# Performance work log

Hardware: AMD Instinct MI355X
Metric: run time of the kernel (lower is better)

The kernel has to match this reference:

```python
import jax, jax.numpy as jnp
import numpy as np

B, T, F = 512, 512, 16
UNITS = [64, 32, 32, 32]
VOCAB, EDIM = 1281, 4


def setup_inputs() -> dict:
    key = jax.random.key(0)
    ks = jax.random.split(key, 32)
    x = jax.random.normal(ks[0], (B, T, F), jnp.float32)
    # column 1 holds integer org ids (stored as float, as in the TF model)
    ids = jax.random.randint(ks[1], (B, T), 0, VOCAB).astype(jnp.float32)
    x = x.at[:, :, 1].set(ids)
    d = {"input_tensor": x,
         "emb": jax.random.normal(ks[2], (VOCAB, EDIM), jnp.float32) * 0.05}
    din = 1 + (F - 2) + EDIM  # 18
    i = 3
    for l, u in enumerate(UNITS):
        d[f"k{l}"] = jax.random.normal(ks[i], (din, 3 * u), jnp.float32) * 0.1; i += 1
        d[f"r{l}"] = jax.random.normal(ks[i], (u, 3 * u), jnp.float32) * 0.1; i += 1
        d[f"bi{l}"] = jnp.zeros((3 * u,), jnp.float32)
        d[f"bh{l}"] = jnp.zeros((3 * u,), jnp.float32)
        din = u
    u = UNITS[-1]
    d["w1"] = jax.random.normal(ks[i], (u, u), jnp.float32) * 0.1; i += 1
    d["b1"] = jnp.zeros((u,), jnp.float32)
    d["w2"] = jax.random.normal(ks[i], (u, u), jnp.float32) * 0.1; i += 1
    d["b2"] = jnp.zeros((u,), jnp.float32)
    d["v"] = jax.random.normal(ks[i], (u, 1), jnp.float32) * 0.1; i += 1
    d["bv"] = jnp.zeros((1,), jnp.float32)
    d["wd"] = jax.random.normal(ks[i], (u, 2), jnp.float32) * 0.1; i += 1
    d["bd"] = jnp.zeros((2,), jnp.float32)
    return d


def _gru(h, xp, rk, bh):
    # Keras GRUCell (reset_after=True). xp = x @ kernel + input_bias, [B, 3u]
    hp = h @ rk + bh
    xz, xr, xh = jnp.split(xp, 3, axis=-1)
    hz, hr, hhp = jnp.split(hp, 3, axis=-1)
    z = jax.nn.sigmoid(xz + hz)
    r = jax.nn.sigmoid(xr + hr)
    hh = jnp.tanh(xh + r * hhp)
    return z * h + (1.0 - z) * hh


def _forward(input_tensor, emb, k0, r0, bi0, bh0, k1, r1, bi1, bh1,
             k2, r2, bi2, bh2, k3, r3, bi3, bh3,
             w1, b1, w2, b2, v, bv, wd, bd):
    f0 = input_tensor[:, :, :1]                      # [B,T,1]
    ids = input_tensor[:, :, 1].astype(jnp.int32)    # [B,T]
    rest = input_tensor[:, :, 2:]                    # [B,T,F-2]
    e = emb[ids]                                     # [B,T,4]
    inp = jnp.concatenate([f0, rest, e], axis=2)     # [B,T,din]

    # precompute layer-0 input projection as one big GEMM
    xp0 = inp @ k0 + bi0                             # [B,T,3*64]
    bsz = inp.shape[0]
    init = tuple(jnp.zeros((bsz, u), inp.dtype) for u in UNITS)

    def step(carry, xp_t):
        h0, h1, h2, h3 = carry
        h0 = _gru(h0, xp_t, r0, bh0)
        h1 = _gru(h1, h0 @ k1 + bi1, r1, bh1)
        h2 = _gru(h2, h1 @ k2 + bi2, r2, bh2)
        h3 = _gru(h3, h2 @ k3 + bi3, r3, bh3)
        return (h0, h1, h2, h3), h3

    (_, _, _, hT), seq = jax.lax.scan(step, init, jnp.swapaxes(xp0, 0, 1))
    outputs = jnp.swapaxes(seq, 0, 1)                # [B,T,32] (last-layer sequence)

    # Bahdanau attention: query = final state of last layer
    score = jnp.tanh(outputs @ w1 + b1 + (hT @ w2 + b2)[:, None, :]) @ v + bv  # [B,T,1]
    attn = jax.nn.softmax(score, axis=1)
    ctx = jnp.sum(attn * outputs, axis=1)            # [B,32]
    return jax.nn.softmax(ctx @ wd + bd, axis=-1)    # [B,2]


def reference(input_tensor, emb, k0, r0, bi0, bh0, k1, r1, bi1, bh1,
              k2, r2, bi2, bh2, k3, r3, bi3, bh3,
              w1, b1, w2, b2, v, bv, wd, bd):
    return _forward(input_tensor, emb, k0, r0, bi0, bh0, k1, r1, bi1, bh1,
                    k2, r2, bi2, bh2, k3, r3, bi3, bh3,
                    w1, b1, w2, b2, v, bv, wd, bd)
```

## Files before the change

### kernel.cpp

```cpp
#include <hip/hip_runtime.h>

#define TLEN 512
#define FIN 16

__device__ __forceinline__ float sigm(float x) { return 1.0f / (1.0f + __expf(-x)); }
__device__ __forceinline__ float tanh_f(float x) {
  x = fminf(fmaxf(x, -15.0f), 15.0f);
  float e = __expf(2.0f * x);
  return (e - 1.0f) / (e + 1.0f);
}

__device__ __forceinline__ float gru_fin(float own_main, float own_xh, float own_hhp,
                                         int role, float hold) {
  const float oth_main = __shfl_xor(own_main, 1);
  const float xh  = own_xh  + __shfl_xor(own_xh, 1);
  const float hhp = own_hhp + __shfl_xor(own_hhp, 1);
  const float sz = role ? oth_main : own_main;
  const float sr = role ? own_main : oth_main;
  const float z = sigm(sz);
  const float r = sigm(sr);
  const float hh = tanh_f(xh + r * hhp);
  return z * hold + (1.f - z) * hh;
}

__global__ __launch_bounds__(256, 1)
void rnn_pipe3(const float* __restrict__ x, const float* __restrict__ emb,
               const float* __restrict__ k0, const float* __restrict__ r0,
               const float* __restrict__ bi0, const float* __restrict__ bh0,
               const float* __restrict__ k1, const float* __restrict__ r1,
               const float* __restrict__ bi1, const float* __restrict__ bh1,
               const float* __restrict__ k2, const float* __restrict__ r2,
               const float* __restrict__ bi2, const float* __restrict__ bh2,
               const float* __restrict__ k3, const float* __restrict__ r3,
               const float* __restrict__ bi3, const float* __restrict__ bh3,
               const float* __restrict__ w1, const float* __restrict__ b1,
               const float* __restrict__ w2, const float* __restrict__ b2,
               const float* __restrict__ vv, const float* __restrict__ bv,
               const float* __restrict__ wd, const float* __restrict__ bd,
               float* __restrict__ out, float* __restrict__ obuf)
{
  __shared__ __align__(16) float s_xin[TLEN][20][2];
  __shared__ __align__(16) float s_h0[2][64][2];
  __shared__ __align__(16) float s_h1[2][32][2];
  __shared__ __align__(16) float s_h2[2][32][2];
  __shared__ __align__(16) float s_h3[2][32][2];
  __shared__ __align__(16) float s_pA[2][64][2];
  __shared__ __align__(16) float s_pAh[2][64][2];
  __shared__ __align__(16) float s_fl[2][16][2][32];
  __shared__ __align__(16) float e_w1[1024];
  __shared__ __align__(16) float e_sc[1024];
  __shared__ float e_hw2[64], e_b1[32], e_v[32], e_ctx[64];

  const int tid  = threadIdx.x;
  const int wid  = tid >> 6;
  const int lane = tid & 63;
  const int g    = lane >> 1;
  const int role = lane & 1;
  const int bb0  = blockIdx.x * 2;

  float Wa[96], Wb[48], Wc[48];
  float bm = 0.f, bxh = 0.f, bhh = 0.f;
  float cbm = 0.f, cbxh = 0.f, cbhh = 0.f;

  if (wid <= 1) {
    const int u  = wid * 32 + g;
    const int cm = role ? 64 + u : u;
    #pragma unroll
    for (int j = 0; j < 19; ++j) Wa[j] = k0[j*192 + cm];
    Wa[19] = 0.f;
    #pragma unroll
    for (int j = 0; j < 64; ++j) Wa[20+j] = r0[j*192 + cm];
    #pragma unroll
    for (int jj = 0; jj < 10; ++jj) {
      const int row = role*10 + jj;
      Wb[jj] = (row < 19) ? k0[row*192 + 128 + u] : 0.f;
    }
    #pragma unroll
    for (int jj = 0; jj < 32; ++jj) Wb[10+jj] = r0[(role*32+jj)*192 + 128 + u];
    bm  = bi0[cm] + bh0[cm];
    bxh = role ? 0.f : bi0[128+u];
    bhh = role ? bh0[128+u] : 0.f;
  }
  if (wid == 0) {
    const int cma = role ? 32 + g : g;
    #pragma unroll
    for (int j = 0; j < 32; ++j) Wc[j] = k3[j*96 + cma];
    #pragma unroll
    for (int jj = 0; jj < 16; ++jj) Wc[32+jj] = k3[(role*16+jj)*96 + 64 + g];
  }
  if (wid == 2) {
    const int cm = role ? 32 + g : g;
    #pragma unroll
    for (int j = 0; j < 64; ++j) Wa[j] = k1[j*96 + cm];
    #pragma unroll
    for (int j = 0; j < 32; ++j) Wa[64+j] = r1[j*96 + cm];
    #pragma unroll
    for (int jj = 0; jj < 32; ++jj) Wb[jj] = k1[(role*32+jj)*96 + 64 + g];
    #pragma unroll
    for (int jj = 0; jj < 16; ++jj) Wb[32+jj] = r1[(role*16+jj)*96 + 64 + g];
    bm  = bi1[cm] + bh1[cm];
    bxh = role ? 0.f : bi1[64+g];
    bhh = role ? bh1[64+g] : 0.f;
  }
  if (wid == 3) {
    const int cm = role ? 32 + g : g;
    #pragma unroll
    for (int j = 0; j < 32; ++j) Wa[j] = k2[j*96 + cm];
    #pragma unroll
    for (int j = 0; j < 32; ++j) Wa[32+j] = r2[j*96 + cm];
    #pragma unroll
    for (int jj = 0; jj < 16; ++jj) Wb[jj] = k2[(role*16+jj)*96 + 64 + g];
    #pragma unroll
    for (int jj = 0; jj < 16; ++jj) Wb[16+jj] = r2[(role*16+jj)*96 + 64 + g];
    bm  = bi2[cm] + bh2[cm];
    bxh = role ? 0.f : bi2[64+g];
    bhh = role ? bh2[64+g] : 0.f;
    #pragma unroll
    for (int j = 0; j < 32; ++j) Wc[j] = r3[j*96 + cm];
    #pragma unroll
    for (int jj = 0; jj < 16; ++jj) Wc[32+jj] = r3[(role*16+jj)*96 + 64 + g];
    cbm  = bi3[cm] + bh3[cm];
    cbxh = bi3[64+g];
    cbhh = bh3[64+g];
  }

  ((float*)s_h0)[tid] = 0.f;
  if (tid < 128) {
    ((float*)s_h1)[tid] = 0.f;
    ((float*)s_h2)[tid] = 0.f;
    ((float*)s_h3)[tid] = 0.f;
  }

  for (int r = tid; r < 2*TLEN; r += 256) {
    const int b2 = r & 1, t2 = r >> 1;
    const float* xr = &x[((size_t)(bb0+b2)*TLEN + t2)*FIN];
    const float4 x0 = *(const float4*)(xr);
    const float4 x1 = *(const float4*)(xr+4);
    const float4 x2 = *(const float4*)(xr+8);
    const float4 x3 = *(const float4*)(xr+12);
    float v[20];
    v[0]=x0.x; v[1]=x0.z; v[2]=x0.w;
    v[3]=x1.x; v[4]=x1.y; v[5]=x1.z; v[6]=x1.w;
    v[7]=x2.x; v[8]=x2.y; v[9]=x2.z; v[10]=x2.w;
    v[11]=x3.x; v[12]=x3.y; v[13]=x3.z; v[14]=x3.w;
    const int id = (int)x0.y;
    const float4 e4 = *(const float4*)&emb[id*4];
    v[15]=e4.x; v[16]=e4.y; v[17]=e4.z; v[18]=e4.w; v[19]=0.f;
    #pragma unroll
    for (int j = 0; j < 20; ++j) s_xin[t2][j][b2] = v[j];
  }

  auto flush = [&](int c) {
    const int par = c & 1;
    #pragma unroll
    for (int it = 0; it < 4; ++it) {
      const int f4 = it*64 + lane;
      const int u4 = f4 & 7, row = f4 >> 3;
      const int dt = row >> 1, b2 = row & 1;
      const float4 vq = *(const float4*)&s_fl[par][dt][b2][u4*4];
      *(float4*)&obuf[(((size_t)(bb0+b2)*TLEN) + c*16 + dt)*32 + u4*4] = vq;
    }
  };

  for (int i = 0; i < 516; ++i) {
    __syncthreads();
    const int wp = i & 1;
    const int rp = wp ^ 1;

    if (wid <= 1) {
      if (i < 512) {
        const int u = wid*32 + g;
        float a0A = bm, a0B = bm, a1A = 0.f, a1B = 0.f;
        #pragma unroll
        for (int j = 0; j < 20; j += 2) {
          const float4 q = *(const float4*)&s_xin[i][j][0];
          a0A += Wa[j]*q.x;   a0B += Wa[j]*q.y;
          a1A += Wa[j+1]*q.z; a1B += Wa[j+1]*q.w;
        }
        #pragma unroll
        for (int j = 0; j < 64; j += 2) {
          const float4 q = *(const float4*)&s_h0[rp][j][0];
          a0A += Wa[20+j]*q.x; a0B += Wa[20+j]*q.y;
          a1A += Wa[21+j]*q.z; a1B += Wa[21+j]*q.w;
        }
        float xqA = bxh, xqB = bxh;
        #pragma unroll
        for (int jj = 0; jj < 10; ++jj) {
          const float2 d = *(const float2*)&s_xin[i][role*10+jj][0];
          xqA += Wb[jj]*d.x; xqB += Wb[jj]*d.y;
        }
        float p0A = bhh, p0B = bhh, p1A = 0.f, p1B = 0.f;
        #pragma unroll
        for (int jj = 0; jj < 32; jj += 2) {
          const float4 q = *(const float4*)&s_h0[rp][role*32+jj][0];
          p0A += Wb[10+jj]*q.x; p0B += Wb[10+jj]*q.y;
          p1A += Wb[11+jj]*q.z; p1B += Wb[11+jj]*q.w;
        }
        const float holdA = s_h0[rp][u][0];
        const float holdB = s_h0[rp][u][1];
        const float hnA = gru_fin(a0A+a1A, xqA, p0A+p1A, role, holdA);
        const float hnB = gru_fin(a0B+a1B, xqB, p0B+p1B, role, holdB);
        if (!role) { s_h0[wp][u][0] = hnA; s_h0[wp][u][1] = hnB; }
      }
      if (wid == 0) {
        if (i >= 3 && i <= 514) {
          float q0A=0.f,q0B=0.f,q1A=0.f,q1B=0.f;
          #pragma unroll
          for (int j = 0; j < 32; j += 2) {
            const float4 q = *(const float4*)&s_h2[rp][j][0];
            q0A += Wc[j]*q.x;   q0B += Wc[j]*q.y;
            q1A += Wc[j+1]*q.z; q1B += Wc[j+1]*q.w;
          }
          float phA=0.f, phB=0.f, ph1A=0.f, ph1B=0.f;
          #pragma unroll
          for (int jj = 0; jj < 16; jj += 2) {
            const float4 q = *(const float4*)&s_h2[rp][role*16+jj][0];
            phA  += Wc[32+jj]*q.x; phB  += Wc[32+jj]*q.y;
            ph1A += Wc[33+jj]*q.z; ph1B += Wc[33+jj]*q.w;
          }
          s_pA[wp][lane][0]  = q0A+q1A;  s_pA[wp][lane][1]  = q0B+q1B;
          s_pAh[wp][lane][0] = phA+ph1A; s_pAh[wp][lane][1] = phB+ph1B;
        }
      } else {
        if (i >= 20 && ((i - 20) & 15) == 0) flush((i - 20) >> 4);
      }
    } else if (wid == 2) {
      if (i >= 1 && i <= 512) {
        float a0A = bm, a0B = bm, a1A=0.f, a1B=0.f;
        #pragma unroll
        for (int j = 0; j < 64; j += 2) {
          const float4 q = *(const float4*)&s_h0[rp][j][0];
          a0A += Wa[j]*q.x;   a0B += Wa[j]*q.y;
          a1A += Wa[j+1]*q.z; a1B += Wa[j+1]*q.w;
        }
        #pragma unroll
        for (int j = 0; j < 32; j += 2) {
          const float4 q = *(const float4*)&s_h1[rp][j][0];
          a0A += Wa[64+j]*q.x; a0B += Wa[64+j]*q.y;
          a1A += Wa[65+j]*q.z; a1B += Wa[65+j]*q.w;
        }
        float x0A = bxh, x0B = bxh, x1A = 0.f, x1B = 0.f;
        #pragma unroll
        for (int jj = 0; jj < 32; jj += 2) {
          const float4 q = *(const float4*)&s_h0[rp][role*32+jj][0];
          x0A += Wb[jj]*q.x;   x0B += Wb[jj]*q.y;
          x1A += Wb[jj+1]*q.z; x1B += Wb[jj+1]*q.w;
        }
        float p0A = bhh, p0B = bhh, p1A = 0.f, p1B = 0.f;
        #pragma unroll
        for (int jj = 0; jj < 16; jj += 2) {
          const float4 q = *(const float4*)&s_h1[rp][role*16+jj][0];
          p0A += Wb[32+jj]*q.x; p0B += Wb[32+jj]*q.y;
          p1A += Wb[33+jj]*q.z; p1B += Wb[33+jj]*q.w;
        }
        const float holdA = s_h1[rp][g][0];
        const float holdB = s_h1[rp][g][1];
        const float hnA = gru_fin(a0A+a1A, x0A+x1A, p0A+p1A, role, holdA);
        const float hnB = gru_fin(a0B+a1B, x0B+x1B, p0B+p1B, role, holdB);
        if (!role) { s_h1[wp][g][0] = hnA; s_h1[wp][g][1] = hnB; }
      }
    } else {
      if (i >= 2 && i <= 513) {
        float a0A = bm, a0B = bm, a1A=0.f, a1B=0.f;
        #pragma unroll
        for (int j = 0; j < 32; j += 2) {
          const float4 q = *(const float4*)&s_h1[rp][j][0];
          a0A += Wa[j]*q.x;   a0B += Wa[j]*q.y;
          a1A += Wa[j+1]*q.z; a1B += Wa[j+1]*q.w;
        }
        #pragma unroll
        for (int j = 0; j < 32; j += 2) {
          const float4 q = *(const float4*)&s_h2[rp][j][0];
          a0A += Wa[32+j]*q.x; a0B += Wa[32+j]*q.y;
          a1A += Wa[33+j]*q.z; a1B += Wa[33+j]*q.w;
        }
        float x0A = bxh, x0B = bxh, x1A = 0.f, x1B = 0.f;
        #pragma unroll
        for (int jj = 0; jj < 16; jj += 2) {
          const float4 q = *(const float4*)&s_h1[rp][role*16+jj][0];
          x0A += Wb[jj]*q.x;   x0B += Wb[jj]*q.y;
          x1A += Wb[jj+1]*q.z; x1B += Wb[jj+1]*q.w;
        }
        float p0A = bhh, p0B = bhh, p1A = 0.f, p1B = 0.f;
        #pragma unroll
        for (int jj = 0; jj < 16; jj += 2) {
          const float4 q = *(const float4*)&s_h2[rp][role*16+jj][0];
          p0A += Wb[16+jj]*q.x; p0B += Wb[16+jj]*q.y;
          p1A += Wb[17+jj]*q.z; p1B += Wb[17+jj]*q.w;
        }
        const float holdA = s_h2[rp][g][0];
        const float holdB = s_h2[rp][g][1];
        const float hnA = gru_fin(a0A+a1A, x0A+x1A, p0A+p1A, role, holdA);
        const float hnB = gru_fin(a0B+a1B, x0B+x1B, p0B+p1B, role, holdB);
        if (!role) { s_h2[wp][g][0] = hnA; s_h2[wp][g][1] = hnB; }
      }
      if (i >= 4) {
        float q0A=0.f,q0B=0.f,q1A=0.f,q1B=0.f;
        #pragma unroll
        for (int jj = 0; jj < 32; jj += 2) {
          const float4 q = *(const float4*)&s_h3[rp][jj][0];
          q0A += Wc[jj]*q.x;   q0B += Wc[jj]*q.y;
          q1A += Wc[jj+1]*q.z; q1B += Wc[jj+1]*q.w;
        }
        float ph0A=0.f, ph0B=0.f, ph1A=0.f, ph1B=0.f;
        #pragma unroll
        for (int jj = 0; jj < 16; jj += 2) {
          const float4 q = *(const float4*)&s_h3[rp][role*16+jj][0];
          ph0A += Wc[32+jj]*q.x; ph0B += Wc[32+jj]*q.y;
          ph1A += Wc[33+jj]*q.z; ph1B += Wc[33+jj]*q.w;
        }
        const float mainA = s_pA[rp][lane][0] + q0A + q1A + cbm;
        const float mainB = s_pA[rp][lane][1] + q0B + q1B + cbm;
        const float xhA_own = s_pAh[rp][lane][0];
        const float xhB_own = s_pAh[rp][lane][1];
        const float phA_own = ph0A + ph1A;
        const float phB_own = ph0B + ph1B;

        const float othA = __shfl_xor(mainA, 1);
        const float othB = __shfl_xor(mainB, 1);
        const float xhA = xhA_own + __shfl_xor(xhA_own, 1) + cbxh;
        const float xhB = xhB_own + __shfl_xor(xhB_own, 1) + cbxh;
        const float hhpA = phA_own + __shfl_xor(phA_own, 1) + cbhh;
        const float hhpB = phB_own + __shfl_xor(phB_own, 1) + cbhh;

        const float szA = role ? othA : mainA;
        const float srA = role ? mainA : othA;
        const float szB = role ? othB : mainB;
        const float srB = role ? mainB : othB;
        const float zA = sigm(szA), rA = sigm(srA);
        const float zB = sigm(szB), rB = sigm(srB);
        const float hhA = tanh_f(xhA + rA*hhpA);
        const float hhB = tanh_f(xhB + rB*hhpB);
        const float hnA = zA*s_h3[rp][g][0] + (1.f-zA)*hhA;
        const float hnB = zB*s_h3[rp][g][1] + (1.f-zB)*hhB;
        if (!role) {
          s_h3[wp][g][0] = hnA;
          s_h3[wp][g][1] = hnB;
          const int t3 = i - 4;
          s_fl[(t3>>4)&1][t3&15][0][g] = hnA;
          s_fl[(t3>>4)&1][t3&15][1][g] = hnB;
        }
      }
    }
  }
  __syncthreads();

  if (wid == 1) flush(31);

  for (int kk = tid; kk < 1024; kk += 256) e_w1[kk] = w1[kk];
  if (tid < 32) { e_b1[tid] = b1[tid]; e_v[tid] = vv[tid]; }
  if (tid >= 64 && tid < 128) {
    const int u = tid & 31, bb = (tid - 64) >> 5;
    float s = b2[u];
    #pragma unroll
    for (int j = 0; j < 32; ++j) s += s_h3[1][j][bb] * w2[j*32 + u];
    e_hw2[bb*32 + u] = s;
  }
  __syncthreads();

  #pragma unroll
  for (int c = 0; c < 4; ++c) {
    const int idx = c*256 + tid;
    const int bb = idx >> 9, t2 = idx & 511;
    const float* row = obuf + ((size_t)(bb0+bb)*TLEN + t2)*32;
    float rr[32];
    #pragma unroll
    for (int j = 0; j < 32; j += 4) {
      const float4 r4 = *(const float4*)&row[j];
      rr[j]=r4.x; rr[j+1]=r4.y; rr[j+2]=r4.z; rr[j+3]=r4.w;
    }
    float sc = 0.f;
    for (int u = 0; u < 32; ++u) {
      float qv = e_b1[u] + e_hw2[bb*32 + u];
      #pragma unroll
      for (int j = 0; j < 32; ++j) qv += rr[j]*e_w1[j*32+u];
      sc += tanh_f(qv)*e_v[u];
    }
    e_sc[idx] = sc;
  }
  __syncthreads();

  {
    if (wid < 2) {
      const int bb = wid;
      float sv[8]; float m = -1e30f;
      #pragma unroll
      for (int k = 0; k < 8; ++k) { sv[k] = e_sc[bb*512 + lane + 64*k]; m = fmaxf(m, sv[k]); }
      #pragma unroll
      for (int off = 32; off > 0; off >>= 1) m = fmaxf(m, __shfl_xor(m, off));
      float ss = 0.f;
      #pragma unroll
      for (int k = 0; k < 8; ++k) { sv[k] = __expf(sv[k]-m); ss += sv[k]; }
      #pragma unroll
      for (int off = 32; off > 0; off >>= 1) ss += __shfl_xor(ss, off);
      const float inv = 1.f/ss;
      #pragma unroll
      for (int k = 0; k < 8; ++k) e_sc[bb*512 + lane + 64*k] = sv[k]*inv;
    }
  }
  __syncthreads();

  if (tid < 64) {
    const int u = tid & 31, bb = tid >> 5;
    float acc = 0.f;
    const float* orow = obuf + (size_t)(bb0+bb)*TLEN*32 + u;
    const float* prow = e_sc + bb*512;
    #pragma unroll 4
    for (int t2 = 0; t2 < 512; ++t2) acc += prow[t2]*orow[(size_t)t2*32];
    e_ctx[bb*32 + u] = acc;
  }
  __syncthreads();

  if (tid < 2) {
    const int bb = tid;
    float l0 = bd[0], l1 = bd[1];
    #pragma unroll
    for (int u = 0; u < 32; ++u) {
      const float cv = e_ctx[bb*32 + u];
      l0 += cv*wd[u*2]; l1 += cv*wd[u*2+1];
    }
    const float mm = fmaxf(l0, l1);
    const float ex0 = __expf(l0-mm), ex1 = __expf(l1-mm);
    const float den = ex0 + ex1;
    out[(bb0+bb)*2 + 0] = ex0/den;
    out[(bb0+bb)*2 + 1] = ex1/den;
  }
}

extern "C" void kernel_launch(void* const* d_in, const int* in_sizes, int n_in,
                              void* d_out, int out_size, void* d_ws, size_t ws_size,
                              hipStream_t stream) {
  const float* x   = (const float*)d_in[0];
  const float* emb = (const float*)d_in[1];
  const float* k0  = (const float*)d_in[2];
  const float* r0  = (const float*)d_in[3];
  const float* bi0 = (const float*)d_in[4];
  const float* bh0 = (const float*)d_in[5];
  const float* k1  = (const float*)d_in[6];
  const float* r1  = (const float*)d_in[7];
  const float* bi1 = (const float*)d_in[8];
  const float* bh1 = (const float*)d_in[9];
  const float* k2  = (const float*)d_in[10];
  const float* r2  = (const float*)d_in[11];
  const float* bi2 = (const float*)d_in[12];
  const float* bh2 = (const float*)d_in[13];
  const float* k3  = (const float*)d_in[14];
  const float* r3  = (const float*)d_in[15];
  const float* bi3 = (const float*)d_in[16];
  const float* bh3 = (const float*)d_in[17];
  const float* w1  = (const float*)d_in[18];
  const float* b1  = (const float*)d_in[19];
  const float* w2  = (const float*)d_in[20];
  const float* b2  = (const float*)d_in[21];
  const float* v   = (const float*)d_in[22];
  const float* bv  = (const float*)d_in[23];
  const float* wd  = (const float*)d_in[24];
  const float* bd  = (const float*)d_in[25];

  float* out  = (float*)d_out;
  float* obuf = (float*)d_ws;

  rnn_pipe3<<<dim3(256), dim3(256), 0, stream>>>(
      x, emb, k0, r0, bi0, bh0, k1, r1, bi1, bh1,
      k2, r2, bi2, bh2, k3, r3, bi3, bh3,
      w1, b1, w2, b2, v, bv, wd, bd, out, obuf);
}
```

Baseline: 1.252 ms.

## Replace per-step block barriers with LDS flag-based dataflow between layer wavefronts

Swaps the lockstep __syncthreads-per-timestep schedule for a producer/consumer dataflow. Each wavefront spins on volatile LDS flags and publishes its progress through an 8-deep ring of hidden-state buffers. The layer-3 work that used to be split across wave 0 and wave 3 now runs entirely in wave 3, and hidden states are carried in registers. This lets layers run ahead of one another instead of waiting on the slowest wave every step. In exchange it adds spin-wait overhead, a longer serial chain in wave 3, and the risk of memory-ordering bugs in the flag protocol.

After: 1.506 ms. 1.2x slower.

```diff
diff --git a/kernel.cpp b/kernel.cpp
--- a/kernel.cpp
+++ b/kernel.cpp
@@ -24,29 +24,28 @@
 }
 
 __global__ __launch_bounds__(256, 1)
-void rnn_pipe3(const float* __restrict__ x, const float* __restrict__ emb,
-               const float* __restrict__ k0, const float* __restrict__ r0,
-               const float* __restrict__ bi0, const float* __restrict__ bh0,
-               const float* __restrict__ k1, const float* __restrict__ r1,
-               const float* __restrict__ bi1, const float* __restrict__ bh1,
-               const float* __restrict__ k2, const float* __restrict__ r2,
-               const float* __restrict__ bi2, const float* __restrict__ bh2,
-               const float* __restrict__ k3, const float* __restrict__ r3,
-               const float* __restrict__ bi3, const float* __restrict__ bh3,
-               const float* __restrict__ w1, const float* __restrict__ b1,
-               const float* __restrict__ w2, const float* __restrict__ b2,
-               const float* __restrict__ vv, const float* __restrict__ bv,
-               const float* __restrict__ wd, const float* __restrict__ bd,
-               float* __restrict__ out, float* __restrict__ obuf)
+void rnn_flow(const float* __restrict__ x, const float* __restrict__ emb,
+              const float* __restrict__ k0, const float* __restrict__ r0,
+              const float* __restrict__ bi0, const float* __restrict__ bh0,
+              const float* __restrict__ k1, const float* __restrict__ r1,
+              const float* __restrict__ bi1, const float* __restrict__ bh1,
+              const float* __restrict__ k2, const float* __restrict__ r2,
+              const float* __restrict__ bi2, const float* __restrict__ bh2,
+              const float* __restrict__ k3, const float* __restrict__ r3,
+              const float* __restrict__ bi3, const float* __restrict__ bh3,
+              const float* __restrict__ w1m, const float* __restrict__ b1,
+              const float* __restrict__ w2m, const float* __restrict__ b2,
+              const float* __restrict__ vv, const float* __restrict__ bv,
+              const float* __restrict__ wd, const float* __restrict__ bd,
+              float* __restrict__ out, float* __restrict__ obuf)
 {
   __shared__ __align__(16) float s_xin[TLEN][20][2];
-  __shared__ __align__(16) float s_h0[2][64][2];
-  __shared__ __align__(16) float s_h1[2][32][2];
-  __shared__ __align__(16) float s_h2[2][32][2];
-  __shared__ __align__(16) float s_h3[2][32][2];
-  __shared__ __align__(16) float s_pA[2][64][2];
-  __shared__ __align__(16) float s_pAh[2][64][2];
-  __shared__ __align__(16) float s_fl[2][16][2][32];
+  __shared__ __align__(16) float s_h0[8][64][2];
+  __shared__ __align__(16) float s_h1[8][32][2];
+  __shared__ __align__(16) float s_h2[8][32][2];
+  __shared__ __align__(16) float s_h3[8][32][2];
+  __shared__ __align__(16) float s_fl[4][16][2][32];
+  __shared__ int s_flag[8];
   __shared__ __align__(16) float e_w1[1024];
   __shared__ __align__(16) float e_sc[1024];
   __shared__ float e_hw2[64], e_b1[32], e_v[32], e_ctx[64];
@@ -58,7 +57,15 @@
   const int role = lane & 1;
   const int bb0  = blockIdx.x * 2;
 
-  float Wa[96], Wb[48], Wc[48];
+#define WAITGE(idx, val) do { volatile int* _f = &s_flag[idx];                 \
+    while (*_f < (val)) {} asm volatile("" ::: "memory"); } while (0)
+#define WAITGE2(i0, i1, val) do { volatile int* _a = &s_flag[i0];              \
+    volatile int* _b = &s_flag[i1];                                            \
+    while (*_a < (val) || *_b < (val)) {} asm volatile("" ::: "memory"); } while (0)
+#define PUBLISH(idx, val) do { asm volatile("s_waitcnt lgkmcnt(0)" ::: "memory"); \
+    if (lane == 0) { *(volatile int*)&s_flag[idx] = (val); } } while (0)
+
+  float W[192];
   float bm = 0.f, bxh = 0.f, bhh = 0.f;
   float cbm = 0.f, cbxh = 0.f, cbhh = 0.f;
 
@@ -66,78 +73,70 @@
     const int u  = wid * 32 + g;
     const int cm = role ? 64 + u : u;
     #pragma unroll
-    for (int j = 0; j < 19; ++j) Wa[j] = k0[j*192 + cm];
-    Wa[19] = 0.f;
-    #pragma unroll
-    for (int j = 0; j < 64; ++j) Wa[20+j] = r0[j*192 + cm];
+    for (int j = 0; j < 19; ++j) W[j] = k0[j*192 + cm];
+    W[19] = 0.f;
+    #pragma unroll
+    for (int j = 0; j < 64; ++j) W[20+j] = r0[j*192 + cm];
     #pragma unroll
     for (int jj = 0; jj < 10; ++jj) {
       const int row = role*10 + jj;
-      Wb[jj] = (row < 19) ? k0[row*192 + 128 + u] : 0.f;
-    }
-    #pragma unroll
-    for (int jj = 0; jj < 32; ++jj) Wb[10+jj] = r0[(role*32+jj)*192 + 128 + u];
+      W[84+jj] = (row < 19) ? k0[row*192 + 128 + u] : 0.f;
+    }
+    #pragma unroll
+    for (int jj = 0; jj < 32; ++jj) W[94+jj] = r0[(role*32+jj)*192 + 128 + u];
     bm  = bi0[cm] + bh0[cm];
     bxh = role ? 0.f : bi0[128+u];
     bhh = role ? bh0[128+u] : 0.f;
-  }
-  if (wid == 0) {
-    const int cma = role ? 32 + g : g;
-    #pragma unroll
-    for (int j = 0; j < 32; ++j) Wc[j] = k3[j*96 + cma];
-    #pragma unroll
-    for (int jj = 0; jj < 16; ++jj) Wc[32+jj] = k3[(role*16+jj)*96 + 64 + g];
-  }
-  if (wid == 2) {
+  } else if (wid == 2) {
     const int cm = role ? 32 + g : g;
     #pragma unroll
-    for (int j = 0; j < 64; ++j) Wa[j] = k1[j*96 + cm];
-    #pragma unroll
-    for (int j = 0; j < 32; ++j) Wa[64+j] = r1[j*96 + cm];
-    #pragma unroll
-    for (int jj = 0; jj < 32; ++jj) Wb[jj] = k1[(role*32+jj)*96 + 64 + g];
-    #pragma unroll
-    for (int jj = 0; jj < 16; ++jj) Wb[32+jj] = r1[(role*16+jj)*96 + 64 + g];
+    for (int j = 0; j < 64; ++j) W[j] = k1[j*96 + cm];
+    #pragma unroll
+    for (int j = 0; j < 32; ++j) W[64+j] = r1[j*96 + cm];
+    #pragma unroll
+    for (int jj = 0; jj < 32; ++jj) W[96+jj]  = k1[(role*32+jj)*96 + 64 + g];
+    #pragma unroll
+    for (int jj = 0; jj < 16; ++jj) W[128+jj] = r1[(role*16+jj)*96 + 64 + g];
     bm  = bi1[cm] + bh1[cm];
     bxh = role ? 0.f : bi1[64+g];
     bhh = role ? bh1[64+g] : 0.f;
-  }
-  if (wid == 3) {
+  } else {
     const int cm = role ? 32 + g : g;
     #pragma unroll
-    for (int j = 0; j < 32; ++j) Wa[j] = k2[j*96 + cm];
-    #pragma unroll
-    for (int j = 0; j < 32; ++j) Wa[32+j] = r2[j*96 + cm];
-    #pragma unroll
-    for (int jj = 0; jj < 16; ++jj) Wb[jj] = k2[(role*16+jj)*96 + 64 + g];
-    #pragma unroll
-    for (int jj = 0; jj < 16; ++jj) Wb[16+jj] = r2[(role*16+jj)*96 + 64 + g];
+    for (int j = 0; j < 32; ++j) { W[j] = k2[j*96 + cm]; W[32+j] = r2[j*96 + cm]; }
+    #pragma unroll
+    for (int jj = 0; jj < 16; ++jj) {
+      W[64+jj] = k2[(role*16+jj)*96 + 64 + g];
+      W[80+jj] = r2[(role*16+jj)*96 + 64 + g];
+    }
+    #pragma unroll
+    for (int j = 0; j < 32; ++j) { W[96+j] = k3[j*96 + cm]; W[128+j] = r3[j*96 + cm]; }
+    #pragma unroll
+    for (int jj = 0; jj < 16; ++jj) {
+      W[160+jj] = k3[(role*16+jj)*96 + 64 + g];
+      W[176+jj] = r3[(role*16+jj)*96 + 64 + g];
+    }
     bm  = bi2[cm] + bh2[cm];
     bxh = role ? 0.f : bi2[64+g];
     bhh = role ? bh2[64+g] : 0.f;
-    #pragma unroll
-    for (int j = 0; j < 32; ++j) Wc[j] = r3[j*96 + cm];
-    #pragma unroll
-    for (int jj = 0; jj < 16; ++jj) Wc[32+jj] = r3[(role*16+jj)*96 + 64 + g];
     cbm  = bi3[cm] + bh3[cm];
     cbxh = bi3[64+g];
     cbhh = bh3[64+g];
   }
 
-  ((float*)s_h0)[tid] = 0.f;
-  if (tid < 128) {
-    ((float*)s_h1)[tid] = 0.f;
-    ((float*)s_h2)[tid] = 0.f;
-    ((float*)s_h3)[tid] = 0.f;
-  }
+  for (int q = tid; q < 1024; q += 256) ((float*)s_h0)[q] = 0.f;
+  for (int q = tid; q < 512; q += 256) {
+    ((float*)s_h1)[q] = 0.f; ((float*)s_h2)[q] = 0.f; ((float*)s_h3)[q] = 0.f;
+  }
+  if (tid < 8) s_flag[tid] = (tid == 4) ? 0 : -1;
 
   for (int r = tid; r < 2*TLEN; r += 256) {
     const int b2 = r & 1, t2 = r >> 1;
-    const float* xr = &x[((size_t)(bb0+b2)*TLEN + t2)*FIN];
+    const float* xr = &x[((size_t)(bb0 + b2) * TLEN + t2) * FIN];
     const float4 x0 = *(const float4*)(xr);
-    const float4 x1 = *(const float4*)(xr+4);
-    const float4 x2 = *(const float4*)(xr+8);
-    const float4 x3 = *(const float4*)(xr+12);
+    const float4 x1 = *(const float4*)(xr + 4);
+    const float4 x2 = *(const float4*)(xr + 8);
+    const float4 x3 = *(const float4*)(xr + 12);
     float v[20];
     v[0]=x0.x; v[1]=x0.z; v[2]=x0.w;
     v[3]=x1.x; v[4]=x1.y; v[5]=x1.z; v[6]=x1.w;
@@ -149,9 +148,10 @@
     #pragma unroll
     for (int j = 0; j < 20; ++j) s_xin[t2][j][b2] = v[j];
   }
+  __syncthreads();
 
   auto flush = [&](int c) {
-    const int par = c & 1;
+    const int par = c & 3;
     #pragma unroll
     for (int it = 0; it < 4; ++it) {
       const int f4 = it*64 + lane;
@@ -162,167 +162,175 @@
     }
   };
 
-  for (int i = 0; i < 516; ++i) {
-    __syncthreads();
-    const int wp = i & 1;
-    const int rp = wp ^ 1;
-
-    if (wid <= 1) {
-      if (i < 512) {
-        const int u = wid*32 + g;
+  if (wid <= 1) {
+    const int u = wid*32 + g;
+    const int FWD = wid ^ 1;
+    float holdA = 0.f, holdB = 0.f;
+    for (int t = 0; t < TLEN; ++t) {
+      if ((t & 3) == 0) WAITGE(2, t - 4);
+      WAITGE(FWD, t - 1);
+      const int sl = t & 7, slp = (t - 1) & 7;
+      float a0A = bm, a0B = bm, a1A = 0.f, a1B = 0.f;
+      #pragma unroll
+      for (int j = 0; j < 20; j += 2) {
+        const float4 q = *(const float4*)&s_xin[t][j][0];
+        a0A += W[j]*q.x;   a0B += W[j]*q.y;
+        a1A += W[j+1]*q.z; a1B += W[j+1]*q.w;
+      }
+      #pragma unroll
+      for (int j = 0; j < 64; j += 2) {
+        const float4 q = *(const float4*)&s_h0[slp][j][0];
+        a0A += W[20+j]*q.x; a0B += W[20+j]*q.y;
+        a1A += W[21+j]*q.z; a1B += W[21+j]*q.w;
+      }
+      float xqA = bxh, xqB = bxh;
+      #pragma unroll
+      for (int jj = 0; jj < 10; ++jj) {
+        const float2 d = *(const float2*)&s_xin[t][role*10+jj][0];
+        xqA += W[84+jj]*d.x; xqB += W[84+jj]*d.y;
+      }
+      float p0A = bhh, p0B = bhh, p1A = 0.f, p1B = 0.f;
+      #pragma unroll
+      for (int jj = 0; jj < 32; jj += 2) {
+        const float4 q = *(const float4*)&s_h0[slp][role*32+jj][0];
+        p0A += W[94+jj]*q.x; p0B += W[94+jj]*q.y;
+        p1A += W[95+jj]*q.z; p1B += W[95+jj]*q.w;
+      }
+      const float hnA = gru_fin(a0A+a1A, xqA, p0A+p1A, role, holdA);
+      const float hnB = gru_fin(a0B+a1B, xqB, p0B+p1B, role, holdB);
+      holdA = hnA; holdB = hnB;
+      if (!role) { s_h0[sl][u][0] = hnA; s_h0[sl][u][1] = hnB; }
+      PUBLISH(wid, t);
+      if (wid == 1 && t >= 20 && ((t - 20) & 15) == 0) {
+        const int c = (t - 20) >> 4;
+        WAITGE(3, 16*c + 16);
+        flush(c);
+        PUBLISH(4, c + 1);
+      }
+    }
+    if (wid == 1) {
+      WAITGE(3, TLEN);
+      flush(31);
+      PUBLISH(4, 32);
+    }
+  } else if (wid == 2) {
+    float holdA = 0.f, holdB = 0.f;
+    for (int t = 0; t < TLEN; ++t) {
+      if ((t & 3) == 0) WAITGE(3, t - 4);
+      WAITGE2(0, 1, t);
+      const int sl = t & 7, slp = (t - 1) & 7;
+      float a0A = bm, a0B = bm, a1A = 0.f, a1B = 0.f;
+      #pragma unroll
+      for (int j = 0; j < 64; j += 2) {
+        const float4 q = *(const float4*)&s_h0[sl][j][0];
+        a0A += W[j]*q.x;   a0B += W[j]*q.y;
+        a1A += W[j+1]*q.z; a1B += W[j+1]*q.w;
+      }
+      #pragma unroll
+      for (int j = 0; j < 32; j += 2) {
+        const float4 q = *(const float4*)&s_h1[slp][j][0];
+        a0A += W[64+j]*q.x; a0B += W[64+j]*q.y;
+        a1A += W[65+j]*q.z; a1B += W[65+j]*q.w;
+      }
+      float x0A = bxh, x0B = bxh, x1A = 0.f, x1B = 0.f;
+      #pragma unroll
+      for (int jj = 0; jj < 32; jj += 2) {
+        const float4 q = *(const float4*)&s_h0[sl][role*32+jj][0];
+        x0A += W[96+jj]*q.x; x0B += W[96+jj]*q.y;
+        x1A += W[97+jj]*q.z; x1B += W[97+jj]*q.w;
+      }
+      float p0A = bhh, p0B = bhh, p1A = 0.f, p1B = 0.f;
+      #pragma unroll
+      for (int jj = 0; jj < 16; jj += 2) {
+        const float4 q = *(const float4*)&s_h1[slp][role*16+jj][0];
+        p0A += W[128+jj]*q.x; p0B += W[128+jj]*q.y;
+        p1A += W[129+jj]*q.z; p1B += W[129+jj]*q.w;
+      }
+      const float hnA = gru_fin(a0A+a1A, x0A+x1A, p0A+p1A, role, holdA);
+      const float hnB = gru_fin(a0B+a1B, x0B+x1B, p0B+p1B, role, holdB);
+      holdA = hnA; holdB = hnB;
+      if (!role) { s_h1[sl][g][0] = hnA; s_h1[sl][g][1] = hnB; }
+      PUBLISH(2, t);
+    }
+  } else {
+    float hold2A = 0.f, hold2B = 0.f, hold3A = 0.f, hold3B = 0.f;
+    for (int j = 0; j <= TLEN; ++j) {
+      if ((j & 15) == 0) WAITGE(4, (j >> 4) - 3);
+      if (j < TLEN) {
+        WAITGE(2, j);
+        const int sl = j & 7, slp = (j - 1) & 7;
         float a0A = bm, a0B = bm, a1A = 0.f, a1B = 0.f;
         #pragma unroll
-        for (int j = 0; j < 20; j += 2) {
-          const float4 q = *(const float4*)&s_xin[i][j][0];
-          a0A += Wa[j]*q.x;   a0B += Wa[j]*q.y;
-          a1A += Wa[j+1]*q.z; a1B += Wa[j+1]*q.w;
-        }
-        #pragma unroll
-        for (int j = 0; j < 64; j += 2) {
-          const float4 q = *(const float4*)&s_h0[rp][j][0];
-          a0A += Wa[20+j]*q.x; a0B += Wa[20+j]*q.y;
-          a1A += Wa[21+j]*q.z; a1B += Wa[21+j]*q.w;
-        }
-        float xqA = bxh, xqB = bxh;
-        #pragma unroll
-        for (int jj = 0; jj < 10; ++jj) {
-          const float2 d = *(const float2*)&s_xin[i][role*10+jj][0];
-          xqA += Wb[jj]*d.x; xqB += Wb[jj]*d.y;
+        for (int jq = 0; jq < 32; jq += 2) {
+          const float4 q = *(const float4*)&s_h1[sl][jq][0];
+          a0A += W[jq]*q.x;   a0B += W[jq]*q.y;
+          a1A += W[jq+1]*q.z; a1B += W[jq+1]*q.w;
+        }
+        #pragma unroll
+        for (int jq = 0; jq < 32; jq += 2) {
+          const float4 q = *(const float4*)&s_h2[slp][jq][0];
+          a0A += W[32+jq]*q.x; a0B += W[32+jq]*q.y;
+          a1A += W[33+jq]*q.z; a1B += W[33+jq]*q.w;
+        }
+        float x0A = bxh, x0B = bxh, x1A = 0.f, x1B = 0.f;
+        #pragma unroll
+        for (int jj = 0; jj < 16; jj += 2) {
+          const float4 q = *(const float4*)&s_h1[sl][role*16+jj][0];
+          x0A += W[64+jj]*q.x; x0B += W[64+jj]*q.y;
+          x1A += W[65+jj]*q.z; x1B += W[65+jj]*q.w;
         }
         float p0A = bhh, p0B = bhh, p1A = 0.f, p1B = 0.f;
         #pragma unroll
-        for (int jj = 0; jj < 32; jj += 2) {
-          const float4 q = *(const float4*)&s_h0[rp][role*32+jj][0];
-          p0A += Wb[10+jj]*q.x; p0B += Wb[10+jj]*q.y;
-          p1A += Wb[11+jj]*q.z; p1B += Wb[11+jj]*q.w;
-        }
-        const float holdA = s_h0[rp][u][0];
-        const float holdB = s_h0[rp][u][1];
-        const float hnA = gru_fin(a0A+a1A, xqA, p0A+p1A, role, holdA);
-        const float hnB = gru_fin(a0B+a1B, xqB, p0B+p1B, role, holdB);
-        if (!role) { s_h0[wp][u][0] = hnA; s_h0[wp][u][1] = hnB; }
-      }
-      if (wid == 0) {
-        if (i >= 3 && i <= 514) {
-          float q0A=0.f,q0B=0.f,q1A=0.f,q1B=0.f;
-          #pragma unroll
-          for (int j = 0; j < 32; j += 2) {
-            const float4 q = *(const float4*)&s_h2[rp][j][0];
-            q0A += Wc[j]*q.x;   q0B += Wc[j]*q.y;
-            q1A += Wc[j+1]*q.z; q1B += Wc[j+1]*q.w;
-          }
-          float phA=0.f, phB=0.f, ph1A=0.f, ph1B=0.f;
-          #pragma unroll
-          for (int jj = 0; jj < 16; jj += 2) {
-            const float4 q = *(const float4*)&s_h2[rp][role*16+jj][0];
-            phA  += Wc[32+jj]*q.x; phB  += Wc[32+jj]*q.y;
-            ph1A += Wc[33+jj]*q.z; ph1B += Wc[33+jj]*q.w;
-          }
-          s_pA[wp][lane][0]  = q0A+q1A;  s_pA[wp][lane][1]  = q0B+q1B;
-          s_pAh[wp][lane][0] = phA+ph1A; s_pAh[wp][lane][1] = phB+ph1B;
-        }
-      } else {
-        if (i >= 20 && ((i - 20) & 15) == 0) flush((i - 20) >> 4);
-      }
-    } else if (wid == 2) {
-      if (i >= 1 && i <= 512) {
-        float a0A = bm, a0B = bm, a1A=0.f, a1B=0.f;
-        #pragma unroll
-        for (int j = 0; j < 64; j += 2) {
-          const float4 q = *(const float4*)&s_h0[rp][j][0];
-          a0A += Wa[j]*q.x;   a0B += Wa[j]*q.y;
-          a1A += Wa[j+1]*q.z; a1B += Wa[j+1]*q.w;
-        }
-        #pragma unroll
-        for (int j = 0; j < 32; j += 2) {
-          const float4 q = *(const float4*)&s_h1[rp][j][0];
-          a0A += Wa[64+j]*q.x; a0B += Wa[64+j]*q.y;
-          a1A += Wa[65+j]*q.z; a1B += Wa[65+j]*q.w;
-        }
-        float x0A = bxh, x0B = bxh, x1A = 0.f, x1B = 0.f;
-        #pragma unroll
-        for (int jj = 0; jj < 32; jj += 2) {
-          const float4 q = *(const float4*)&s_h0[rp][role*32+jj][0];
-          x0A += Wb[jj]*q.x;   x0B += Wb[jj]*q.y;
-          x1A += Wb[jj+1]*q.z; x1B += Wb[jj+1]*q.w;
-        }
-        float p0A = bhh, p0B = bhh, p1A = 0.f, p1B = 0.f;
-        #pragma unroll
         for (int jj = 0; jj < 16; jj += 2) {
-          const float4 q = *(const float4*)&s_h1[rp][role*16+jj][0];
-          p0A += Wb[32+jj]*q.x; p0B += Wb[32+jj]*q.y;
-          p1A += Wb[33+jj]*q.z; p1B += Wb[33+jj]*q.w;
-        }
-        const float holdA = s_h1[rp][g][0];
-        const float holdB = s_h1[rp][g][1];
-        const float hnA = gru_fin(a0A+a1A, x0A+x1A, p0A+p1A, role, holdA);
-        const float hnB = gru_fin(a0B+a1B, x0B+x1B, p0B+p1B, role, holdB);
-        if (!role) { s_h1[wp][g][0] = hnA; s_h1[wp][g][1] = hnB; }
-      }
-    } else {
-      if (i >= 2 && i <= 513) {
-        float a0A = bm, a0B = bm, a1A=0.f, a1B=0.f;
-        #pragma unroll
-        for (int j = 0; j < 32; j += 2) {
-          const float4 q = *(const float4*)&s_h1[rp][j][0];
-          a0A += Wa[j]*q.x;   a0B += Wa[j]*q.y;
-          a1A += Wa[j+1]*q.z; a1B += Wa[j+1]*q.w;
-        }
-        #pragma unroll
-        for (int j = 0; j < 32; j += 2) {
-          const float4 q = *(const float4*)&s_h2[rp][j][0];
-          a0A += Wa[32+j]*q.x; a0B += Wa[32+j]*q.y;
-          a1A += Wa[33+j]*q.z; a1B += Wa[33+j]*q.w;
-        }
-        float x0A = bxh, x0B = bxh, x1A = 0.f, x1B = 0.f;
+          const float4 q = *(const float4*)&s_h2[slp][role*16+jj][0];
+          p0A += W[80+jj]*q.x; p0B += W[80+jj]*q.y;
+          p1A += W[81+jj]*q.z; p1B += W[81+jj]*q.w;
+        }
+        const float hnA = gru_fin(a0A+a1A, x0A+x1A, p0A+p1A, role, hold2A);
+        const float hnB = gru_fin(a0B+a1B, x0B+x1B, p0B+p1B, role, hold2B);
+        hold2A = hnA; hold2B = hnB;
+        if (!role) { s_h2[sl][g][0] = hnA; s_h2[sl][g][1] = hnB; }
+      }
+      if (j >= 1) {
+        const int t3 = j - 1;
+        const int s3 = t3 & 7, s3p = (t3 - 1) & 7;
+        float q0A=0.f,q0B=0.f,q1A=0.f,q1B=0.f;
+        #pragma unroll
+        for (int jq = 0; jq < 32; jq += 2) {
+          const float4 q = *(const float4*)&s_h2[s3][jq][0];
+          q0A += W[96+jq]*q.x; q0B += W[96+jq]*q.y;
+          q1A += W[97+jq]*q.z; q1B += W[97+jq]*q.w;
+        }
+        #pragma unroll
+        for (int jq = 0; jq < 32; jq += 2) {
+          const float4 q = *(const float4*)&s_h3[s3p][jq][0];
+          q0A += W[128+jq]*q.x; q0B += W[128+jq]*q.y;
+          q1A += W[129+jq]*q.z; q1B += W[129+jq]*q.w;
+        }
+        float xh0A=0.f,xh0B=0.f,xh1A=0.f,xh1B=0.f;
         #pragma unroll
         for (int jj = 0; jj < 16; jj += 2) {
-          const float4 q = *(const float4*)&s_h1[rp][role*16+jj][0];
-          x0A += Wb[jj]*q.x;   x0B += Wb[jj]*q.y;
-          x1A += Wb[jj+1]*q.z; x1B += Wb[jj+1]*q.w;
-        }
-        float p0A = bhh, p0B = bhh, p1A = 0.f, p1B = 0.f;
+          const float4 q = *(const float4*)&s_h2[s3][role*16+jj][0];
+          xh0A += W[160+jj]*q.x; xh0B += W[160+jj]*q.y;
+          xh1A += W[161+jj]*q.z; xh1B += W[161+jj]*q.w;
+        }
+        float ph0A=0.f,ph0B=0.f,ph1A=0.f,ph1B=0.f;
         #pragma unroll
         for (int jj = 0; jj < 16; jj += 2) {
-          const float4 q = *(const float4*)&s_h2[rp][role*16+jj][0];
-          p0A += Wb[16+jj]*q.x; p0B += Wb[16+jj]*q.y;
-          p1A += Wb[17+jj]*q.z; p1B += Wb[17+jj]*q.w;
-        }
-        const float holdA = s_h2[rp][g][0];
-        const float holdB = s_h2[rp][g][1];
-        const float hnA = gru_fin(a0A+a1A, x0A+x1A, p0A+p1A, role, holdA);
-        const float hnB = gru_fin(a0B+a1B, x0B+x1B, p0B+p1B, role, holdB);
-        if (!role) { s_h2[wp][g][0] = hnA; s_h2[wp][g][1] = hnB; }
-      }
-      if (i >= 4) {
-        float q0A=0.f,q0B=0.f,q1A=0.f,q1B=0.f;
-        #pragma unroll
-        for (int jj = 0; jj < 32; jj += 2) {
-          const float4 q = *(const float4*)&s_h3[rp][jj][0];
-          q0A += Wc[jj]*q.x;   q0B += Wc[jj]*q.y;
-          q1A += Wc[jj+1]*q.z; q1B += Wc[jj+1]*q.w;
-        }
-        float ph0A=0.f, ph0B=0.f, ph1A=0.f, ph1B=0.f;
-        #pragma unroll
-        for (int jj = 0; jj < 16; jj += 2) {
-          const float4 q = *(const float4*)&s_h3[rp][role*16+jj][0];
-          ph0A += Wc[32+jj]*q.x; ph0B += Wc[32+jj]*q.y;
-          ph1A += Wc[33+jj]*q.z; ph1B += Wc[33+jj]*q.w;
-        }
-        const float mainA = s_pA[rp][lane][0] + q0A + q1A + cbm;
-        const float mainB = s_pA[rp][lane][1] + q0B + q1B + cbm;
-        const float xhA_own = s_pAh[rp][lane][0];
-        const float xhB_own = s_pAh[rp][lane][1];
-        const float phA_own = ph0A + ph1A;
-        const float phB_own = ph0B + ph1B;
-
+          const float4 q = *(const float4*)&s_h3[s3p][role*16+jj][0];
+          ph0A += W[176+jj]*q.x; ph0B += W[176+jj]*q.y;
+          ph1A += W[177+jj]*q.z; ph1B += W[177+jj]*q.w;
+        }
+        const float mainA = q0A + q1A + cbm;
+        const float mainB = q0B + q1B + cbm;
+        const float xhAo = xh0A + xh1A, xhBo = xh0B + xh1B;
+        const float phAo = ph0A + ph1A, phBo = ph0B + ph1B;
         const float othA = __shfl_xor(mainA, 1);
         const float othB = __shfl_xor(mainB, 1);
-        const float xhA = xhA_own + __shfl_xor(xhA_own, 1) + cbxh;
-        const float xhB = xhB_own + __shfl_xor(xhB_own, 1) + cbxh;
-        const float hhpA = phA_own + __shfl_xor(phA_own, 1) + cbhh;
-        const float hhpB = phB_own + __shfl_xor(phB_own, 1) + cbhh;
-
+        const float xhA = xhAo + __shfl_xor(xhAo, 1) + cbxh;
+        const float xhB = xhBo + __shfl_xor(xhBo, 1) + cbxh;
+        const float hhpA = phAo + __shfl_xor(phAo, 1) + cbhh;
+        const float hhpB = phBo + __shfl_xor(phBo, 1) + cbhh;
         const float szA = role ? othA : mainA;
         const float srA = role ? mainA : othA;
         const float szB = role ? othB : mainB;
@@ -331,29 +339,27 @@
         const float zB = sigm(szB), rB = sigm(srB);
         const float hhA = tanh_f(xhA + rA*hhpA);
         const float hhB = tanh_f(xhB + rB*hhpB);
-        const float hnA = zA*s_h3[rp][g][0] + (1.f-zA)*hhA;
-        const float hnB = zB*s_h3[rp][g][1] + (1.f-zB)*hhB;
+        const float hnA = zA*hold3A + (1.f-zA)*hhA;
+        const float hnB = zB*hold3B + (1.f-zB)*hhB;
+        hold3A = hnA; hold3B = hnB;
         if (!role) {
-          s_h3[wp][g][0] = hnA;
-          s_h3[wp][g][1] = hnB;
-          const int t3 = i - 4;
-          s_fl[(t3>>4)&1][t3&15][0][g] = hnA;
-          s_fl[(t3>>4)&1][t3&15][1][g] = hnB;
-        }
-      }
-    }
-  }
-  __syncthreads();
-
-  if (wid == 1) flush(31);
-
-  for (int kk = tid; kk < 1024; kk += 256) e_w1[kk] = w1[kk];
+          s_h3[s3][g][0] = hnA; s_h3[s3][g][1] = hnB;
+          s_fl[(t3>>4)&3][t3&15][0][g] = hnA;
+          s_fl[(t3>>4)&3][t3&15][1][g] = hnB;
+        }
+      }
+      PUBLISH(3, j);
+    }
+  }
+  __syncthreads();
+
+  for (int kk = tid; kk < 1024; kk += 256) e_w1[kk] = w1m[kk];
   if (tid < 32) { e_b1[tid] = b1[tid]; e_v[tid] = vv[tid]; }
   if (tid >= 64 && tid < 128) {
     const int u = tid & 31, bb = (tid - 64) >> 5;
     float s = b2[u];
     #pragma unroll
-    for (int j = 0; j < 32; ++j) s += s_h3[1][j][bb] * w2[j*32 + u];
+    for (int j = 0; j < 32; ++j) s += s_h3[7][j][bb] * w2m[j*32 + u];
     e_hw2[bb*32 + u] = s;
   }
   __syncthreads();
@@ -425,6 +431,9 @@
     out[(bb0+bb)*2 + 0] = ex0/den;
     out[(bb0+bb)*2 + 1] = ex1/den;
   }
+#undef WAITGE
+#undef WAITGE2
+#undef PUBLISH
 }
 
 extern "C" void kernel_launch(void* const* d_in, const int* in_sizes, int n_in,
@@ -460,7 +469,7 @@
   float* out  = (float*)d_out;
   float* obuf = (float*)d_ws;
 
-  rnn_pipe3<<<dim3(256), dim3(256), 0, stream>>>(
+  rnn_flow<<<dim3(256), dim3(256), 0, stream>>>(
       x, emb, k0, r0, bi0, bh0, k1, r1, bi1, bh1,
       k2, r2, bi2, bh2, k3, r3, bi3, bh3,
       w1, b1, w2, b2, v, bv, wd, bd, out, obuf);
```
